# Kernel tuning notes

Measured on AMD Instinct MI355X. Metric: run time of the kernel, lower is better.

## Reference

```python
import jax, jax.numpy as jnp
import numpy as np

BS, N, D, B, D_PM = 8, 4096, 1024, 8, 64
BUDGET = 16.0


def setup_inputs() -> dict:
    key = jax.random.key(0)
    ks = jax.random.split(key, 6)
    H = jax.random.normal(ks[0], (BS, N, D), jnp.float32)
    surprise = jax.random.normal(ks[1], (BS, N, D), jnp.float32)
    # W_pm initialized as (1/B)*I + small noise, as in initialize()
    eye = jnp.eye(D_PM, dtype=jnp.float32)
    W_pm = eye / B + 0.01 * jax.random.normal(ks[2], (BS, B, D_PM, D_PM), jnp.float32)
    proj_in_w = jax.random.normal(ks[3], (D_PM, D), jnp.float32) / np.float32(np.sqrt(D))
    proj_in_b = jnp.zeros((D_PM,), jnp.float32)
    # original zero-inits proj_out; use small values so output is non-trivial
    proj_out_w = 0.02 * jax.random.normal(ks[4], (D, D_PM), jnp.float32)
    proj_out_b = jnp.zeros((D,), jnp.float32)
    raw_beta = jnp.full((B,), -3.0, jnp.float32)
    raw_decay = jnp.full((B,), np.float32(np.log(0.999 / 0.001)), jnp.float32)  # logit(0.999)
    surp_scale = jnp.ones((1,), jnp.float32)
    surp_bias = jnp.zeros((1,), jnp.float32)
    return dict(H=H, surprise=surprise, W_pm=W_pm,
                proj_in_w=proj_in_w, proj_in_b=proj_in_b,
                proj_out_w=proj_out_w, proj_out_b=proj_out_b,
                raw_beta=raw_beta, raw_decay=raw_decay,
                surp_scale=surp_scale, surp_bias=surp_bias)


def reference(H, surprise, W_pm, proj_in_w, proj_in_b, proj_out_w, proj_out_b,
              raw_beta, raw_decay, surp_scale, surp_bias):
    # ---- read ----
    pre = jnp.einsum('bnd,pd->bnp', H, proj_in_w) + proj_in_b          # [BS,N,D_pm]
    W_sum = jnp.sum(W_pm, axis=1)                                      # [BS,D_pm,D_pm]
    post = jnp.einsum('bnp,bqp->bnq', pre, W_sum)                      # pre @ W_sum^T
    pm_read = jnp.einsum('bnq,dq->bnd', post, proj_out_w) + proj_out_b # [BS,N,D]
    # ---- commit (Hebbian, surprise-gated) ----
    surp_mag = jnp.linalg.norm(surprise, axis=-1)                      # [BS,N]
    s = jax.nn.sigmoid(surp_scale * surp_mag + surp_bias)              # [BS,N]
    weighted = jnp.sqrt(s)[..., None] * pre                            # [BS,N,D_pm]
    G = jnp.einsum('bnp,bnq->bpq', weighted, weighted) / N             # [BS,D_pm,D_pm]
    beta = jax.nn.softplus(raw_beta)                                   # [B]
    decay = jax.nn.sigmoid(raw_decay)                                  # [B]
    eye = jnp.eye(D_PM, dtype=pre.dtype)
    T = decay[None, :, None, None] * eye + beta[None, :, None, None] * G[:, None]  # [BS,B,D_pm,D_pm]
    W_new = jnp.einsum('bkij,bkjq->bkiq', W_pm, T)                     # [BS,B,D_pm,D_pm]
    frob = jnp.sqrt(jnp.sum(W_new * W_new, axis=(-2, -1), keepdims=True))
    scale = jnp.minimum(BUDGET / jnp.maximum(frob, 1e-8), 1.0)
    W_new = W_new * scale
    return pm_read, W_new
```

## Files before the change

### kernel.cpp

```cpp
#include <hip/hip_runtime.h>

typedef unsigned short u16;
typedef unsigned int u32;
typedef __attribute__((ext_vector_type(4))) float f32x4;
typedef __attribute__((ext_vector_type(8))) short s16x8;

static constexpr int N_ = 4096;
static constexpr int D_ = 1024;

#define WAITV(N) asm volatile("s_waitcnt vmcnt(" #N ")" ::: "memory")
#define MEMCLOB() asm volatile("" ::: "memory")

__device__ __forceinline__ u16 f2bf(float f) {
  unsigned u = __float_as_uint(f);
  u += 0x7FFFu + ((u >> 16) & 1u);
  return (u16)(u >> 16);
}

__device__ __forceinline__ f32x4 zero4() {
  f32x4 z; z[0] = 0.f; z[1] = 0.f; z[2] = 0.f; z[3] = 0.f; return z;
}

__device__ __forceinline__ void gload16(const void* g, void* lds) {
  __builtin_amdgcn_global_load_lds(
      (const __attribute__((address_space(1))) u32*)g,
      (__attribute__((address_space(3))) u32*)lds, 16, 0, 0);
}

__global__ __launch_bounds__(256) void k_aux(
    const float* __restrict__ Wpm, const float* __restrict__ piw,
    const float* __restrict__ pw, const float* __restrict__ Sur,
    const float* __restrict__ sscale_p, const float* __restrict__ sbias_p,
    u16* __restrict__ WpB, u16* __restrict__ MB, float* __restrict__ sqs_ws) {
  __shared__ float Ws[64][65];
  int bid = blockIdx.x, tid = threadIdx.x;
  if (bid < 16) {
    size_t i0 = (size_t)bid * 4096;
    for (int idx = tid; idx < 4096; idx += 256)
      WpB[i0 + idx] = f2bf(piw[i0 + idx]);
    return;
  }
  if (bid < 144) {
    int idx2 = bid - 16;
    int b = idx2 >> 4, t = idx2 & 15;
    for (int idx = tid; idx < 4096; idx += 256) {
      float s = 0.f;
#pragma unroll
      for (int k = 0; k < 8; ++k)
        s += Wpm[((size_t)(b * 8 + k)) * 4096 + idx];
      Ws[idx >> 6][idx & 63] = s;
    }
    __syncthreads();
    u16* mb = MB + ((size_t)b << 16);
    for (int oidx = tid; oidx < 4096; oidx += 256) {
      int r = oidx >> 6, c = oidx & 63;
      int drow = t * 64 + r;
      const float* prow = pw + (size_t)drow * 64;
      float acc = 0.f;
#pragma unroll 8
      for (int q = 0; q < 64; ++q) acc += prow[q] * Ws[q][c];
      mb[(size_t)drow * 64 + c] = f2bf(acc);
    }
    return;
  }
  int w = tid >> 6, lane = tid & 63;
  int fr = (bid - 144) * 16 + w * 4;
  const float4* r0 = (const float4*)(Sur + (size_t)fr * 1024) + lane;
  float s0 = 0.f, s1 = 0.f, s2 = 0.f, s3 = 0.f;
#pragma unroll
  for (int c = 0; c < 4; ++c) {
    float4 v0 = r0[c * 64];
    float4 v1 = r0[256 + c * 64];
    float4 v2 = r0[512 + c * 64];
    float4 v3 = r0[768 + c * 64];
    s0 += v0.x * v0.x + v0.y * v0.y + v0.z * v0.z + v0.w * v0.w;
    s1 += v1.x * v1.x + v1.y * v1.y + v1.z * v1.z + v1.w * v1.w;
    s2 += v2.x * v2.x + v2.y * v2.y + v2.z * v2.z + v2.w * v2.w;
    s3 += v3.x * v3.x + v3.y * v3.y + v3.z * v3.z + v3.w * v3.w;
  }
#pragma unroll
  for (int m = 1; m < 64; m <<= 1) {
    s0 += __shfl_xor(s0, m, 64);
    s1 += __shfl_xor(s1, m, 64);
    s2 += __shfl_xor(s2, m, 64);
    s3 += __shfl_xor(s3, m, 64);
  }
  float res = s0;
  if (lane == 1) res = s1;
  if (lane == 2) res = s2;
  if (lane == 3) res = s3;
  if (lane < 4) {
    float mag = sqrtf(res);
    float s = 1.f / (1.f + __expf(-(sscale_p[0] * mag + sbias_p[0])));
    sqs_ws[fr + lane] = sqrtf(s);
  }
}

__global__ __launch_bounds__(512, 4) void k_main(
    const float* __restrict__ H, const float* __restrict__ pib,
    const float* __restrict__ pob, const u16* __restrict__ WpB,
    const u16* __restrict__ MB, const float* __restrict__ sqs_ws,
    float* __restrict__ Gpart, float* __restrict__ out) {
  __shared__ __align__(16) char arena[65536];

  const int tid = threadIdx.x;
  const int lane = tid & 63;
  const int w = tid >> 6;
  const int wm = w & 3;
  const int wk = w >> 2;
  const int llo = lane & 15;
  const int lhi = lane >> 4;
  const int b = blockIdx.x >> 6;
  const int row0 = (blockIdx.x & 63) * 64;

  float bias_t[4];
#pragma unroll
  for (int t = 0; t < 4; ++t) bias_t[t] = pib[t * 16 + llo];
  float sqs_r[4];
#pragma unroll
  for (int r = 0; r < 4; ++r)
    sqs_r[r] = sqs_ws[b * 4096 + row0 + wm * 16 + lhi * 4 + r];

  const int c16 = (lane & 7) ^ (lane >> 3);
  const float* hsrc0 = H + ((size_t)b * N_ + row0 + wm * 16 + (lane >> 3)) * D_ +
                       wk * 512 + c16 * 4;
  const float* hsrc1 = hsrc0 + 8 * D_;
  char* wbase = arena + w * 2048;
  const u16* wpb = WpB + (size_t)wk * 512 + lhi * 8;

  f32x4 accA[4];
#pragma unroll
  for (int t = 0; t < 4; ++t) accA[t] = zero4();
  s16x8 Bf[2][4];

#define STAGEH(kc)                                                     \
  gload16(hsrc0 + (kc) * 32, wbase + ((kc) & 3) * 16384);              \
  gload16(hsrc1 + (kc) * 32, wbase + ((kc) & 3) * 16384 + 1024)

#define LOADB(kc)                                                      \
  _Pragma("unroll") for (int t = 0; t < 4; ++t) Bf[(kc) & 1][t] =      \
      *(const s16x8*)(wpb + (size_t)(t * 16 + llo) * 1024 + (kc) * 32)

  STAGEH(0); MEMCLOB();
  LOADB(0);  MEMCLOB();
  STAGEH(1); MEMCLOB();
  LOADB(1);  MEMCLOB();
  STAGEH(2); MEMCLOB();

  const int jblk = (llo >> 3) * 1024;
  const int r7 = llo & 7;
  const int slot_lo = r7 * 8 + ((lhi * 2) ^ r7);
  const int slot_hi = r7 * 8 + ((lhi * 2 + 1) ^ r7);

#pragma unroll
  for (int kc = 0; kc < 16; ++kc) {
    if (kc <= 13) { WAITV(8); }
    else if (kc == 14) { WAITV(6); }
    else { WAITV(0); }
    {
      const char* base = arena + (kc & 3) * 16384 + w * 2048 + jblk;
      f32x4 alo = *(const f32x4*)(base + slot_lo * 16);
      f32x4 ahi = *(const f32x4*)(base + slot_hi * 16);
      s16x8 af;
      af[0] = (short)f2bf(alo[0]); af[1] = (short)f2bf(alo[1]);
      af[2] = (short)f2bf(alo[2]); af[3] = (short)f2bf(alo[3]);
      af[4] = (short)f2bf(ahi[0]); af[5] = (short)f2bf(ahi[1]);
      af[6] = (short)f2bf(ahi[2]); af[7] = (short)f2bf(ahi[3]);
#pragma unroll
      for (int t = 0; t < 4; ++t)
        accA[t] = __builtin_amdgcn_mfma_f32_16x16x32_bf16(af, Bf[kc & 1][t],
                                                          accA[t], 0, 0, 0);
    }
    MEMCLOB();
    if (kc + 2 < 16) { LOADB(kc + 2); }
    MEMCLOB();
    if (kc + 3 < 16) { STAGEH(kc + 3); }
    MEMCLOB();
  }
#undef STAGEH
#undef LOADB

  __syncthreads();
  float (*preF)[65] = (float(*)[65])arena;
  u16 (*preRP)[72] = (u16(*)[72])(arena + 18432);
  u16 (*wRPT)[72] = (u16(*)[72])(arena + 28672);
  float* pobL = (float*)(arena + 38912);

  if (wk == 1) {
#pragma unroll
    for (int t = 0; t < 4; ++t)
#pragma unroll
      for (int r = 0; r < 4; ++r)
        preF[wm * 16 + lhi * 4 + r][t * 16 + llo] = accA[t][r];
  }
  __syncthreads();
  if (wk == 0) {
#pragma unroll
    for (int t = 0; t < 4; ++t)
#pragma unroll
      for (int r = 0; r < 4; ++r) {
        int row = wm * 16 + lhi * 4 + r;
        float v = accA[t][r] + preF[row][t * 16 + llo] + bias_t[t];
        preRP[row][t * 16 + llo] = f2bf(v);
        wRPT[t * 16 + llo][row] = f2bf(v * sqs_r[r]);
      }
  }
  __syncthreads();

  {
    f32x4 accG[4];
#pragma unroll
    for (int t = 0; t < 4; ++t) accG[t] = zero4();
    s16x8 ag = *(const s16x8*)&wRPT[wm * 16 + llo][wk * 32 + lhi * 8];
#pragma unroll
    for (int t = 0; t < 4; ++t) {
      s16x8 bg = *(const s16x8*)&wRPT[t * 16 + llo][wk * 32 + lhi * 8];
      accG[t] = __builtin_amdgcn_mfma_f32_16x16x32_bf16(ag, bg, accG[t], 0, 0, 0);
    }
    float* gout = Gpart + ((size_t)blockIdx.x * 2 + wk) * 4096;
#pragma unroll
    for (int t = 0; t < 4; ++t)
#pragma unroll
      for (int r = 0; r < 4; ++r)
        gout[(wm * 16 + lhi * 4 + r) * 64 + t * 16 + llo] = accG[t][r];
  }
  pobL[tid] = pob[tid];
  pobL[tid + 512] = pob[tid + 512];
  __syncthreads();

  {
    s16x8 ad0 = *(const s16x8*)&preRP[wm * 16 + llo][lhi * 8];
    s16x8 ad1 = *(const s16x8*)&preRP[wm * 16 + llo][32 + lhi * 8];
    const u16* mcol = MB + ((size_t)b << 16) + (size_t)(wk * 512) * 64 + lhi * 8;
    float* orow = out + ((size_t)b * N_ + row0 + wm * 16) * D_;
#pragma unroll
    for (int c = 0; c < 8; ++c) {
      s16x8 f0[4], f1[4];
#pragma unroll
      for (int i = 0; i < 4; ++i) {
        const u16* p = mcol + (size_t)(c * 64 + i * 16 + llo) * 64;
        f0[i] = *(const s16x8*)p;
        f1[i] = *(const s16x8*)(p + 32);
      }
#pragma unroll
      for (int i = 0; i < 4; ++i) {
        f32x4 acc = zero4();
        acc = __builtin_amdgcn_mfma_f32_16x16x32_bf16(ad0, f0[i], acc, 0, 0, 0);
        acc = __builtin_amdgcn_mfma_f32_16x16x32_bf16(ad1, f1[i], acc, 0, 0, 0);
        int n0 = wk * 512 + c * 64 + i * 16;
        float bias = pobL[n0 + llo];
#pragma unroll
        for (int r = 0; r < 4; ++r)
          orow[(size_t)(lhi * 4 + r) * D_ + n0 + llo] = acc[r] + bias;
      }
    }
  }
}

__global__ __launch_bounds__(256) void k_gred(
    const float* __restrict__ Gpart, float* __restrict__ Gsum) {
  __shared__ float red[4][64];
  int b = blockIdx.x >> 6, g = blockIdx.x & 63;
  int lane = threadIdx.x & 63, q = threadIdx.x >> 6;
  const float* src = Gpart + ((size_t)b * 128 + q * 32) * 4096 + g * 64 + lane;
  float s = 0.f;
#pragma unroll 8
  for (int i = 0; i < 32; ++i) s += src[(size_t)i * 4096];
  red[q][lane] = s;
  __syncthreads();
  if (q == 0)
    Gsum[(size_t)b * 4096 + g * 64 + lane] =
        red[0][lane] + red[1][lane] + red[2][lane] + red[3][lane];
}

__global__ __launch_bounds__(256) void k_wnew(
    const float* __restrict__ Wpm, const float* __restrict__ Gsum,
    const float* __restrict__ rbeta, const float* __restrict__ rdecay,
    float* __restrict__ outW) {
  __shared__ float Wk[64][66];
  __shared__ float Gl[64][66];
  __shared__ float red[4];
  int bk = blockIdx.x;
  int b = bk >> 3, k = bk & 7;
  int tid = threadIdx.x;
  const float* wsrc = Wpm + (size_t)bk * 4096;
  const float* gsrc = Gsum + (size_t)b * 4096;
  for (int idx = tid; idx < 4096; idx += 256) {
    Wk[idx >> 6][idx & 63] = wsrc[idx];
    Gl[idx >> 6][idx & 63] = gsrc[idx];
  }
  __syncthreads();
  float beta = log1pf(__expf(rbeta[k]));
  float decay = 1.f / (1.f + __expf(-rdecay[k]));
  float bn = beta * (1.f / 4096.f);
  int q = tid & 63;
  int rbase = tid >> 6;
  float vals[16];
  float ss = 0.f;
#pragma unroll
  for (int i = 0; i < 16; ++i) {
    int row = i * 4 + rbase;
    float acc = 0.f;
#pragma unroll 8
    for (int j = 0; j < 64; ++j) acc += Wk[row][j] * Gl[j][q];
    float v = decay * Wk[row][q] + bn * acc;
    vals[i] = v;
    ss += v * v;
  }
#pragma unroll
  for (int m = 1; m < 64; m <<= 1) ss += __shfl_xor(ss, m, 64);
  if ((tid & 63) == 0) red[tid >> 6] = ss;
  __syncthreads();
  float frob = sqrtf(red[0] + red[1] + red[2] + red[3]);
  float scale = fminf(16.f / fmaxf(frob, 1e-8f), 1.f);
  float* dst = outW + (size_t)bk * 4096;
#pragma unroll
  for (int i = 0; i < 16; ++i) dst[i * 256 + tid] = vals[i] * scale;
}

extern "C" void kernel_launch(void* const* d_in, const int* in_sizes, int n_in,
                              void* d_out, int out_size, void* d_ws, size_t ws_size,
                              hipStream_t stream) {
  const float* H      = (const float*)d_in[0];
  const float* Sur    = (const float*)d_in[1];
  const float* Wpm    = (const float*)d_in[2];
  const float* piw    = (const float*)d_in[3];
  const float* pib    = (const float*)d_in[4];
  const float* pw     = (const float*)d_in[5];
  const float* pob    = (const float*)d_in[6];
  const float* rbeta  = (const float*)d_in[7];
  const float* rdecay = (const float*)d_in[8];
  const float* sscale = (const float*)d_in[9];
  const float* sbias  = (const float*)d_in[10];
  float* out = (float*)d_out;

  char* ws = (char*)d_ws;
  u16* WpB      = (u16*)(ws);
  u16* MB       = (u16*)(ws + 131072);
  float* sqs_ws = (float*)(ws + 1179648);
  float* Gsum   = (float*)(ws + 1310720);
  float* Gpart  = (float*)(ws + 1441792);

  k_aux<<<2192, 256, 0, stream>>>(Wpm, piw, pw, Sur, sscale, sbias,
                                  WpB, MB, sqs_ws);
  k_main<<<512, 512, 0, stream>>>(H, pib, pob, WpB, MB, sqs_ws, Gpart, out);
  k_gred<<<512, 256, 0, stream>>>(Gpart, Gsum);
  k_wnew<<<64, 256, 0, stream>>>(Wpm, Gsum, rbeta, rdecay,
                                 out + (size_t)8 * 4096 * 1024);
}
```

Before: 160.9 us.

## Shrink k_main tiles to 16 rows with 4-way K split and bf16 G partials

k_main now launches 2048 blocks of 256 threads, each handling 16 rows, where each of the 4 waves covers a quarter of K. Partials are reduced through a smaller LDS arena and the H prefetch depth drops from 3 to 2 stages, which lowers LDS use so more blocks can be resident. Gram partials are stored as bf16, and the per-block count doubles. The output MFMA swaps operands so each lane writes contiguous float4 with a vectorized bias load. Risks include less latency hiding from the shallower pipeline, more G-partial traffic, and some precision loss from the bf16 partial sums.

```diff
diff --git a/kernel.cpp b/kernel.cpp
--- a/kernel.cpp
+++ b/kernel.cpp
@@ -4,6 +4,7 @@
 typedef unsigned int u32;
 typedef __attribute__((ext_vector_type(4))) float f32x4;
 typedef __attribute__((ext_vector_type(8))) short s16x8;
+typedef __attribute__((ext_vector_type(4))) short s16x4;
 
 static constexpr int N_ = 4096;
 static constexpr int D_ = 1024;
@@ -16,11 +17,12 @@
   u += 0x7FFFu + ((u >> 16) & 1u);
   return (u16)(u >> 16);
 }
-
+__device__ __forceinline__ float bf2f(u16 v) {
+  return __uint_as_float((u32)v << 16);
+}
 __device__ __forceinline__ f32x4 zero4() {
   f32x4 z; z[0] = 0.f; z[1] = 0.f; z[2] = 0.f; z[3] = 0.f; return z;
 }
-
 __device__ __forceinline__ void gload16(const void* g, void* lds) {
   __builtin_amdgcn_global_load_lds(
       (const __attribute__((address_space(1))) u32*)g,
@@ -96,22 +98,20 @@
   }
 }
 
-__global__ __launch_bounds__(512, 4) void k_main(
+__global__ __launch_bounds__(256, 6) void k_main(
     const float* __restrict__ H, const float* __restrict__ pib,
     const float* __restrict__ pob, const u16* __restrict__ WpB,
     const u16* __restrict__ MB, const float* __restrict__ sqs_ws,
-    float* __restrict__ Gpart, float* __restrict__ out) {
-  __shared__ __align__(16) char arena[65536];
+    u16* __restrict__ GpartB, float* __restrict__ out) {
+  __shared__ __align__(16) char arena[20096];
 
   const int tid = threadIdx.x;
   const int lane = tid & 63;
   const int w = tid >> 6;
-  const int wm = w & 3;
-  const int wk = w >> 2;
   const int llo = lane & 15;
   const int lhi = lane >> 4;
-  const int b = blockIdx.x >> 6;
-  const int row0 = (blockIdx.x & 63) * 64;
+  const int b = blockIdx.x >> 8;
+  const int row0 = (blockIdx.x & 255) * 16;
 
   float bias_t[4];
 #pragma unroll
@@ -119,14 +119,14 @@
   float sqs_r[4];
 #pragma unroll
   for (int r = 0; r < 4; ++r)
-    sqs_r[r] = sqs_ws[b * 4096 + row0 + wm * 16 + lhi * 4 + r];
+    sqs_r[r] = sqs_ws[b * 4096 + row0 + lhi * 4 + r];
 
   const int c16 = (lane & 7) ^ (lane >> 3);
-  const float* hsrc0 = H + ((size_t)b * N_ + row0 + wm * 16 + (lane >> 3)) * D_ +
-                       wk * 512 + c16 * 4;
+  const float* hsrc0 =
+      H + ((size_t)b * N_ + row0 + (lane >> 3)) * D_ + w * 256 + c16 * 4;
   const float* hsrc1 = hsrc0 + 8 * D_;
   char* wbase = arena + w * 2048;
-  const u16* wpb = WpB + (size_t)wk * 512 + lhi * 8;
+  const u16* wpb = WpB + w * 256 + lhi * 8;
 
   f32x4 accA[4];
 #pragma unroll
@@ -134,8 +134,8 @@
   s16x8 Bf[2][4];
 
 #define STAGEH(kc)                                                     \
-  gload16(hsrc0 + (kc) * 32, wbase + ((kc) & 3) * 16384);              \
-  gload16(hsrc1 + (kc) * 32, wbase + ((kc) & 3) * 16384 + 1024)
+  gload16(hsrc0 + (kc) * 32, wbase + ((kc) & 1) * 8192);               \
+  gload16(hsrc1 + (kc) * 32, wbase + ((kc) & 1) * 8192 + 1024)
 
 #define LOADB(kc)                                                      \
   _Pragma("unroll") for (int t = 0; t < 4; ++t) Bf[(kc) & 1][t] =      \
@@ -145,7 +145,6 @@
   LOADB(0);  MEMCLOB();
   STAGEH(1); MEMCLOB();
   LOADB(1);  MEMCLOB();
-  STAGEH(2); MEMCLOB();
 
   const int jblk = (llo >> 3) * 1024;
   const int r7 = llo & 7;
@@ -153,12 +152,10 @@
   const int slot_hi = r7 * 8 + ((lhi * 2 + 1) ^ r7);
 
 #pragma unroll
-  for (int kc = 0; kc < 16; ++kc) {
-    if (kc <= 13) { WAITV(8); }
-    else if (kc == 14) { WAITV(6); }
-    else { WAITV(0); }
+  for (int kc = 0; kc < 8; ++kc) {
+    if (kc <= 6) { WAITV(6); } else { WAITV(0); }
     {
-      const char* base = arena + (kc & 3) * 16384 + w * 2048 + jblk;
+      const char* base = arena + (kc & 1) * 8192 + w * 2048 + jblk;
       f32x4 alo = *(const f32x4*)(base + slot_lo * 16);
       f32x4 ahi = *(const f32x4*)(base + slot_hi * 16);
       s16x8 af;
@@ -172,69 +169,71 @@
                                                           accA[t], 0, 0, 0);
     }
     MEMCLOB();
-    if (kc + 2 < 16) { LOADB(kc + 2); }
-    MEMCLOB();
-    if (kc + 3 < 16) { STAGEH(kc + 3); }
-    MEMCLOB();
+    if (kc + 2 < 8) { LOADB(kc + 2); MEMCLOB(); STAGEH(kc + 2); MEMCLOB(); }
   }
 #undef STAGEH
 #undef LOADB
 
   __syncthreads();
-  float (*preF)[65] = (float(*)[65])arena;
-  u16 (*preRP)[72] = (u16(*)[72])(arena + 18432);
-  u16 (*wRPT)[72] = (u16(*)[72])(arena + 28672);
-  float* pobL = (float*)(arena + 38912);
-
-  if (wk == 1) {
+  float* preF = (float*)arena;
+  u16* preRP = (u16*)(arena + 12672);
+  u16* wRPT = (u16*)(arena + 14976);
+
+  if (w > 0) {
 #pragma unroll
     for (int t = 0; t < 4; ++t)
 #pragma unroll
       for (int r = 0; r < 4; ++r)
-        preF[wm * 16 + lhi * 4 + r][t * 16 + llo] = accA[t][r];
-  }
-  __syncthreads();
-  if (wk == 0) {
+        preF[(w - 1) * 1056 + (lhi * 4 + r) * 66 + t * 16 + llo] = accA[t][r];
+  }
+  __syncthreads();
+  if (w == 0) {
 #pragma unroll
     for (int t = 0; t < 4; ++t)
 #pragma unroll
       for (int r = 0; r < 4; ++r) {
-        int row = wm * 16 + lhi * 4 + r;
-        float v = accA[t][r] + preF[row][t * 16 + llo] + bias_t[t];
-        preRP[row][t * 16 + llo] = f2bf(v);
-        wRPT[t * 16 + llo][row] = f2bf(v * sqs_r[r]);
+        int row = lhi * 4 + r;
+        int col = t * 16 + llo;
+        float v = accA[t][r] + preF[row * 66 + col] +
+                  preF[1056 + row * 66 + col] + preF[2112 + row * 66 + col] +
+                  bias_t[t];
+        preRP[row * 72 + col] = f2bf(v);
+        wRPT[col * 40 + row] = f2bf(v * sqs_r[r]);
       }
   }
-  __syncthreads();
-
   {
+    int p = tid >> 2, q = tid & 3;
+    s16x4 z4; z4[0] = 0; z4[1] = 0; z4[2] = 0; z4[3] = 0;
+    *(s16x4*)&wRPT[p * 40 + 16 + q * 4] = z4;
+  }
+  __syncthreads();
+
+  {
+    s16x8 ag = *(const s16x8*)&wRPT[(w * 16 + llo) * 40 + lhi * 8];
     f32x4 accG[4];
 #pragma unroll
-    for (int t = 0; t < 4; ++t) accG[t] = zero4();
-    s16x8 ag = *(const s16x8*)&wRPT[wm * 16 + llo][wk * 32 + lhi * 8];
-#pragma unroll
-    for (int t = 0; t < 4; ++t) {
-      s16x8 bg = *(const s16x8*)&wRPT[t * 16 + llo][wk * 32 + lhi * 8];
-      accG[t] = __builtin_amdgcn_mfma_f32_16x16x32_bf16(ag, bg, accG[t], 0, 0, 0);
-    }
-    float* gout = Gpart + ((size_t)blockIdx.x * 2 + wk) * 4096;
-#pragma unroll
-    for (int t = 0; t < 4; ++t)
+    for (int t1 = 0; t1 < 4; ++t1) {
+      s16x8 bg = *(const s16x8*)&wRPT[(t1 * 16 + llo) * 40 + lhi * 8];
+      accG[t1] =
+          __builtin_amdgcn_mfma_f32_16x16x32_bf16(ag, bg, zero4(), 0, 0, 0);
+    }
+    u16* gout = GpartB + (size_t)blockIdx.x * 4096;
+#pragma unroll
+    for (int t1 = 0; t1 < 4; ++t1)
 #pragma unroll
       for (int r = 0; r < 4; ++r)
-        gout[(wm * 16 + lhi * 4 + r) * 64 + t * 16 + llo] = accG[t][r];
-  }
-  pobL[tid] = pob[tid];
-  pobL[tid + 512] = pob[tid + 512];
-  __syncthreads();
+        gout[(w * 16 + lhi * 4 + r) * 64 + t1 * 16 + llo] = f2bf(accG[t1][r]);
+  }
 
   {
-    s16x8 ad0 = *(const s16x8*)&preRP[wm * 16 + llo][lhi * 8];
-    s16x8 ad1 = *(const s16x8*)&preRP[wm * 16 + llo][32 + lhi * 8];
-    const u16* mcol = MB + ((size_t)b << 16) + (size_t)(wk * 512) * 64 + lhi * 8;
-    float* orow = out + ((size_t)b * N_ + row0 + wm * 16) * D_;
-#pragma unroll
-    for (int c = 0; c < 8; ++c) {
+    s16x8 ad0 = *(const s16x8*)&preRP[llo * 72 + lhi * 8];
+    s16x8 ad1 = *(const s16x8*)&preRP[llo * 72 + 32 + lhi * 8];
+    const u16* mcol =
+        MB + ((size_t)b << 16) + (size_t)(w * 256) * 64 + lhi * 8;
+    float* orow = out + ((size_t)b * N_ + row0 + llo) * D_ + w * 256;
+    const float* pobw = pob + w * 256;
+#pragma unroll
+    for (int c = 0; c < 4; ++c) {
       s16x8 f0[4], f1[4];
 #pragma unroll
       for (int i = 0; i < 4; ++i) {
@@ -245,27 +244,30 @@
 #pragma unroll
       for (int i = 0; i < 4; ++i) {
         f32x4 acc = zero4();
-        acc = __builtin_amdgcn_mfma_f32_16x16x32_bf16(ad0, f0[i], acc, 0, 0, 0);
-        acc = __builtin_amdgcn_mfma_f32_16x16x32_bf16(ad1, f1[i], acc, 0, 0, 0);
-        int n0 = wk * 512 + c * 64 + i * 16;
-        float bias = pobL[n0 + llo];
-#pragma unroll
-        for (int r = 0; r < 4; ++r)
-          orow[(size_t)(lhi * 4 + r) * D_ + n0 + llo] = acc[r] + bias;
+        acc = __builtin_amdgcn_mfma_f32_16x16x32_bf16(f0[i], ad0, acc, 0, 0, 0);
+        acc = __builtin_amdgcn_mfma_f32_16x16x32_bf16(f1[i], ad1, acc, 0, 0, 0);
+        int n0 = c * 64 + i * 16 + lhi * 4;
+        float4 bias4 = *(const float4*)&pobw[n0];
+        float4 o;
+        o.x = acc[0] + bias4.x;
+        o.y = acc[1] + bias4.y;
+        o.z = acc[2] + bias4.z;
+        o.w = acc[3] + bias4.w;
+        *(float4*)(orow + n0) = o;
       }
     }
   }
 }
 
 __global__ __launch_bounds__(256) void k_gred(
-    const float* __restrict__ Gpart, float* __restrict__ Gsum) {
+    const u16* __restrict__ GpartB, float* __restrict__ Gsum) {
   __shared__ float red[4][64];
   int b = blockIdx.x >> 6, g = blockIdx.x & 63;
   int lane = threadIdx.x & 63, q = threadIdx.x >> 6;
-  const float* src = Gpart + ((size_t)b * 128 + q * 32) * 4096 + g * 64 + lane;
+  const u16* src = GpartB + ((size_t)(b * 256 + q * 64)) * 4096 + g * 64 + lane;
   float s = 0.f;
 #pragma unroll 8
-  for (int i = 0; i < 32; ++i) s += src[(size_t)i * 4096];
+  for (int i = 0; i < 64; ++i) s += bf2f(src[(size_t)i * 4096]);
   red[q][lane] = s;
   __syncthreads();
   if (q == 0)
@@ -339,12 +341,12 @@
   u16* MB       = (u16*)(ws + 131072);
   float* sqs_ws = (float*)(ws + 1179648);
   float* Gsum   = (float*)(ws + 1310720);
-  float* Gpart  = (float*)(ws + 1441792);
+  u16* GpartB   = (u16*)(ws + 1441792);
 
   k_aux<<<2192, 256, 0, stream>>>(Wpm, piw, pw, Sur, sscale, sbias,
                                   WpB, MB, sqs_ws);
-  k_main<<<512, 512, 0, stream>>>(H, pib, pob, WpB, MB, sqs_ws, Gpart, out);
-  k_gred<<<512, 256, 0, stream>>>(Gpart, Gsum);
+  k_main<<<2048, 256, 0, stream>>>(H, pib, pob, WpB, MB, sqs_ws, GpartB, out);
+  k_gred<<<512, 256, 0, stream>>>(GpartB, Gsum);
   k_wnew<<<64, 256, 0, stream>>>(Wpm, Gsum, rbeta, rdecay,
                                  out + (size_t)8 * 4096 * 1024);
 }
```

After: 198.0 us. 1.23x slower.
